# Kernel optimization log

Hardware: AMD Instinct MI355X
Metric: run time of the kernel (lower is better)

## Reference

```python
import jax, jax.numpy as jnp
import numpy as np
from jax import lax

VOL, PATCH, DIM, DEPTH, HEADS, DIM_HEAD, MLP, CH, B = 64, 8, 768, 4, 12, 64, 3072, 1, 2
INNER = HEADS * DIM_HEAD
GS = VOL // PATCH              # 8 -> N = 512 tokens
EPS = 1e-5


def _sincos_1d(embed_dim, pos):
    omega = np.arange(embed_dim // 2, dtype=float) / (embed_dim / 2.0)
    omega = 1.0 / 10000 ** omega
    out = np.einsum('m,d->md', pos.reshape(-1), omega)
    return np.concatenate([np.sin(out), np.cos(out)], axis=1)


def _pos_embed_3d(embed_dim, gs):
    gd = np.arange(gs, dtype=np.float32)
    gh = np.arange(gs, dtype=np.float32)
    gw = np.arange(gs, dtype=np.float32)
    grid = np.stack(np.meshgrid(gw, gh, gd), axis=0).reshape([3, 1, gs, gs, gs])
    emb = np.concatenate([_sincos_1d(embed_dim // 3, grid[i]) for i in range(3)], axis=1)
    return jnp.asarray(emb, jnp.float32)[None]  # [1, N, dim]


def setup_inputs() -> dict:
    key = jax.random.key(0)
    ks = jax.random.split(key, 12)
    s = 0.02  # xavier-like small init scale
    d = {
        'volume': jax.random.normal(ks[0], (B, CH, VOL, VOL, VOL), jnp.float32),
        'conv_w': jax.random.normal(ks[1], (DIM, CH, PATCH, PATCH, PATCH), jnp.float32) * s,
        'conv_b': jnp.zeros((DIM,), jnp.float32),
        'pos_embed': _pos_embed_3d(DIM, GS),
        'ln1_w': jnp.ones((DEPTH, DIM), jnp.float32),
        'ln1_b': jnp.zeros((DEPTH, DIM), jnp.float32),
        'w_qkv': jax.random.normal(ks[2], (DEPTH, DIM, 3 * INNER), jnp.float32) * s,
        'w_o': jax.random.normal(ks[3], (DEPTH, INNER, DIM), jnp.float32) * s,
        'b_o': jnp.zeros((DEPTH, DIM), jnp.float32),
        'ln2_w': jnp.ones((DEPTH, DIM), jnp.float32),
        'ln2_b': jnp.zeros((DEPTH, DIM), jnp.float32),
        'w1': jax.random.normal(ks[4], (DEPTH, DIM, MLP), jnp.float32) * s,
        'b1': jnp.zeros((DEPTH, MLP), jnp.float32),
        'w2': jax.random.normal(ks[5], (DEPTH, MLP, DIM), jnp.float32) * s,
        'b2': jnp.zeros((DEPTH, DIM), jnp.float32),
        'lnf_w': jnp.ones((DIM,), jnp.float32),
        'lnf_b': jnp.zeros((DIM,), jnp.float32),
    }
    return d


def _ln(x, w, b):
    m = jnp.mean(x, axis=-1, keepdims=True)
    v = jnp.mean(jnp.square(x - m), axis=-1, keepdims=True)
    return (x - m) * lax.rsqrt(v + EPS) * w + b


def _forward(volume, conv_w, conv_b, pos_embed, ln1_w, ln1_b, w_qkv, w_o, b_o,
             ln2_w, ln2_b, w1, b1, w2, b2, lnf_w, lnf_b):
    # Conv3d patch embedding (stride == kernel == patch)
    x = lax.conv_general_dilated(volume, conv_w, window_strides=(PATCH,) * 3,
                                 padding='VALID',
                                 dimension_numbers=('NCDHW', 'OIDHW', 'NCDHW'))
    x = x + conv_b[None, :, None, None, None]
    b = x.shape[0]
    x = x.reshape(b, DIM, -1).transpose(0, 2, 1)   # b (d h w) c -> [B, N, dim]
    x = x + pos_embed
    scale = DIM_HEAD ** -0.5

    def layer(x, p):
        l1w, l1b, wqkv, wo, bo, l2w, l2b, W1, B1, W2, B2 = p
        h = _ln(x, l1w, l1b)
        qkv = h @ wqkv                               # [B, N, 3*inner]
        q, k, v = jnp.split(qkv, 3, axis=-1)
        def heads(t):
            bsz, n, _ = t.shape
            return t.reshape(bsz, n, HEADS, DIM_HEAD).transpose(0, 2, 1, 3)
        q, k, v = heads(q), heads(k), heads(v)
        attn = jax.nn.softmax(jnp.einsum('bhqd,bhkd->bhqk', q, k) * scale, axis=-1)
        o = jnp.einsum('bhqk,bhkd->bhqd', attn, v)   # [B, H, N, dh]
        o = o.transpose(0, 2, 1, 3).reshape(x.shape[0], -1, INNER)
        x = x + (o @ wo + bo)
        h = _ln(x, l2w, l2b)
        x = x + (jnp.tanh(h @ W1 + B1) @ W2 + B2)
        return x, None

    params = (ln1_w, ln1_b, w_qkv, w_o, b_o, ln2_w, ln2_b, w1, b1, w2, b2)
    x, _ = lax.scan(layer, x, params)
    return _ln(x, lnf_w, lnf_b)


def reference(volume, conv_w, conv_b, pos_embed, ln1_w, ln1_b, w_qkv, w_o, b_o,
              ln2_w, ln2_b, w1, b1, w2, b2, lnf_w, lnf_b):
    return _forward(volume, conv_w, conv_b, pos_embed, ln1_w, ln1_b, w_qkv, w_o, b_o,
                    ln2_w, ln2_b, w1, b1, w2, b2, lnf_w, lnf_b)
```

## Files before the change

kernel.cpp:

```cpp
#include <hip/hip_runtime.h>
#include <hip/hip_bf16.h>

typedef __hip_bfloat16 bf16;
typedef short bf16x8 __attribute__((ext_vector_type(8)));
typedef float f32x4 __attribute__((ext_vector_type(4)));

__device__ __forceinline__ float b2f(bf16 v) { return __bfloat162float(v); }
__device__ __forceinline__ void storev(float* p, float v) { *p = v; }
__device__ __forceinline__ void storev(bf16* p, float v) { *p = __float2bfloat16(v); }

__device__ __forceinline__ void gl2lds16(const bf16* g, bf16* l) {
  __builtin_amdgcn_global_load_lds(
      (const __attribute__((address_space(1))) unsigned int*)g,
      (__attribute__((address_space(3))) unsigned int*)l, 16, 0, 0);
}

__global__ void im2col_kernel(const float* __restrict__ vol, bf16* __restrict__ out) {
  int t = blockIdx.x;
  int b = t >> 9, n = t & 511;
  int pd = n >> 6, ph = (n >> 3) & 7, pw = n & 7;
  const float* vb = vol + ((size_t)b << 18);
  for (int l = threadIdx.x; l < 512; l += 256) {
    int i = l >> 6, j = (l >> 3) & 7, k = l & 7;
    out[(size_t)t * 512 + l] =
        __float2bfloat16(vb[(pd * 8 + i) * 4096 + (ph * 8 + j) * 64 + (pw * 8 + k)]);
  }
}

__global__ void convert_kernel(const float* __restrict__ in, bf16* __restrict__ out, int n) {
  int i = (blockIdx.x * 256 + threadIdx.x) * 4;
  if (i + 3 < n) {
    float4 v = *(const float4*)&in[i];
    out[i + 0] = __float2bfloat16(v.x);
    out[i + 1] = __float2bfloat16(v.y);
    out[i + 2] = __float2bfloat16(v.z);
    out[i + 3] = __float2bfloat16(v.w);
  }
}

__global__ __launch_bounds__(256) void transpose_all(
    const float* __restrict__ wqkv, const float* __restrict__ wo,
    const float* __restrict__ w1, const float* __restrict__ w2,
    bf16* __restrict__ tqkv, bf16* __restrict__ two,
    bf16* __restrict__ t1, bf16* __restrict__ t2) {
  int bid = blockIdx.x;
  size_t L = blockIdx.y;
  const float* in;
  bf16* out;
  int R, C, tc, t0;
  if (bid < 432)       { in = wqkv + L * 768 * 2304; out = tqkv + L * 768 * 2304; R = 768;  C = 2304; tc = 36; t0 = bid; }
  else if (bid < 576)  { in = wo + L * 768 * 768;    out = two + L * 768 * 768;   R = 768;  C = 768;  tc = 12; t0 = bid - 432; }
  else if (bid < 1152) { in = w1 + L * 768 * 3072;   out = t1 + L * 768 * 3072;   R = 768;  C = 3072; tc = 48; t0 = bid - 576; }
  else                 { in = w2 + L * 3072 * 768;   out = t2 + L * 3072 * 768;   R = 3072; C = 768;  tc = 12; t0 = bid - 1152; }
  int r0 = (t0 / tc) * 64, c0 = (t0 % tc) * 64;
  __shared__ float tile[64][65];
  int tx = threadIdx.x & 15, ty = threadIdx.x >> 4;
#pragma unroll
  for (int yy = 0; yy < 4; ++yy) {
    float4 v = *(const float4*)&in[(size_t)(r0 + ty + yy * 16) * C + c0 + tx * 4];
    tile[ty + yy * 16][tx * 4 + 0] = v.x;
    tile[ty + yy * 16][tx * 4 + 1] = v.y;
    tile[ty + yy * 16][tx * 4 + 2] = v.z;
    tile[ty + yy * 16][tx * 4 + 3] = v.w;
  }
  __syncthreads();
  int cl = threadIdx.x >> 3;
  int rb = (threadIdx.x & 7) * 8;
#pragma unroll
  for (int half = 0; half < 2; ++half) {
    int c = cl + half * 32;
    bf16 pk[8];
#pragma unroll
    for (int e = 0; e < 8; ++e) pk[e] = __float2bfloat16(tile[rb + e][c]);
    *(uint4*)&out[(size_t)(c0 + c) * R + r0 + rb] = *(uint4*)pk;
  }
}

template <typename OutT>
__global__ void ln_kernel(const float* __restrict__ x, const float* __restrict__ w,
                          const float* __restrict__ b, OutT* __restrict__ out) {
  int row = blockIdx.x, tid = threadIdx.x;
  const float* xr = x + (size_t)row * 768;
  float s = 0.f, ss = 0.f;
  for (int i = tid; i < 768; i += 256) { float v = xr[i]; s += v; ss += v * v; }
  for (int off = 32; off; off >>= 1) {
    s += __shfl_xor(s, off);
    ss += __shfl_xor(ss, off);
  }
  __shared__ float sb[4], ssb[4];
  int wid = tid >> 6;
  if ((tid & 63) == 0) { sb[wid] = s; ssb[wid] = ss; }
  __syncthreads();
  s = sb[0] + sb[1] + sb[2] + sb[3];
  ss = ssb[0] + ssb[1] + ssb[2] + ssb[3];
  float m = s * (1.f / 768.f);
  float var = ss * (1.f / 768.f) - m * m;
  float r = rsqrtf(var + 1e-5f);
  for (int i = tid; i < 768; i += 256)
    storev(out + (size_t)row * 768 + i, (xr[i] - m) * r * w[i] + b[i]);
}

template <int BM, int BN, int EPI>
__global__ __launch_bounds__(256) void mfma_gemm(
    const bf16* __restrict__ A, const bf16* __restrict__ Bt,
    const float* __restrict__ bias, const float* __restrict__ aux,
    bf16* __restrict__ vt,
    void* __restrict__ Cout, int M, int N, int K) {
  constexpr int WTM = BM / 2, WTN = BN / 2;
  constexpr int MT = WTM / 16, NT = WTN / 16;
  __shared__ bf16 As[BM * 64];
  __shared__ bf16 Bs[BN * 64];
  int tid = threadIdx.x;
  int wave = tid >> 6, lane = tid & 63;
  int wm = wave >> 1, wn = wave & 1;
  int m15 = lane & 15, q = lane >> 4;
  int m0 = blockIdx.y * BM, n0 = blockIdx.x * BN;
  int kspan = K / gridDim.z;
  int kbeg = blockIdx.z * kspan, kend = kbeg + kspan;

  f32x4 acc[MT][NT];
#pragma unroll
  for (int i = 0; i < MT; ++i)
#pragma unroll
    for (int j = 0; j < NT; ++j) acc[i][j] = (f32x4){0.f, 0.f, 0.f, 0.f};

  for (int k0 = kbeg; k0 < kend; k0 += 64) {
#pragma unroll
    for (int it = 0; it < BM * 8 / 256; ++it) {
      int c = tid + it * 256;
      int row = c >> 3, cc = c & 7;
      gl2lds16(&A[(size_t)(m0 + row) * K + k0 + cc * 8], &As[c * 8]);
    }
#pragma unroll
    for (int it = 0; it < BN * 8 / 256; ++it) {
      int c = tid + it * 256;
      int row = c >> 3, cc = c & 7;
      gl2lds16(&Bt[(size_t)(n0 + row) * K + k0 + cc * 8], &Bs[c * 8]);
    }
    __syncthreads();
#pragma unroll
    for (int s = 0; s < 2; ++s) {
      bf16x8 af[MT], bfr[NT];
#pragma unroll
      for (int i = 0; i < MT; ++i)
        af[i] = *(const bf16x8*)&As[(wm * WTM + i * 16 + m15) * 64 + s * 32 + q * 8];
#pragma unroll
      for (int j = 0; j < NT; ++j)
        bfr[j] = *(const bf16x8*)&Bs[(wn * WTN + j * 16 + m15) * 64 + s * 32 + q * 8];
#pragma unroll
      for (int i = 0; i < MT; ++i)
#pragma unroll
        for (int j = 0; j < NT; ++j)
          acc[i][j] = __builtin_amdgcn_mfma_f32_16x16x32_bf16(af[i], bfr[j], acc[i][j], 0, 0, 0);
    }
    __syncthreads();
  }

#pragma unroll
  for (int i = 0; i < MT; ++i) {
#pragma unroll
    for (int j = 0; j < NT; ++j) {
      int col = n0 + wn * WTN + j * 16 + m15;
      if (EPI == 4) {
        if (col < 1536) {
#pragma unroll
          for (int r = 0; r < 4; ++r) {
            int row = m0 + wm * WTM + i * 16 + q * 4 + r;
            ((bf16*)Cout)[(size_t)row * 1536 + col] = __float2bfloat16(acc[i][j][r]);
          }
        } else {
          int row0 = m0 + wm * WTM + i * 16 + q * 4;
          int cl = col - 1536;
          int hh = cl >> 6, dd = cl & 63;
          int bb = row0 >> 9, tok = row0 & 511;
          bf16 pk[4];
#pragma unroll
          for (int r = 0; r < 4; ++r) pk[r] = __float2bfloat16(acc[i][j][r]);
          *(uint2*)&vt[((size_t)(bb * 12 + hh) * 64 + dd) * 512 + tok] = *(uint2*)pk;
        }
      } else if (EPI == 5) {
        float bv = (blockIdx.z == 0) ? bias[col] : 0.f;
#pragma unroll
        for (int r = 0; r < 4; ++r) {
          int row = m0 + wm * WTM + i * 16 + q * 4 + r;
          unsafeAtomicAdd(&((float*)Cout)[(size_t)row * N + col], acc[i][j][r] + bv);
        }
      } else {
        float bv = (EPI == 0) ? 0.f : bias[col];
#pragma unroll
        for (int r = 0; r < 4; ++r) {
          int row = m0 + wm * WTM + i * 16 + q * 4 + r;
          float v = acc[i][j][r] + bv;
          if (EPI == 2) v = tanhf(v);
          if (EPI == 3) v += aux[(size_t)(row & 511) * N + col];
          if (EPI == 0 || EPI == 2)
            ((bf16*)Cout)[(size_t)row * N + col] = __float2bfloat16(v);
          else
            ((float*)Cout)[(size_t)row * N + col] = v;
        }
      }
    }
  }
}

__global__ __launch_bounds__(128) void attn_mfma(const bf16* __restrict__ qk,
                                                 const bf16* __restrict__ Vt,
                                                 bf16* __restrict__ o) {
  constexpr int PS = 520;
  __shared__ bf16 KVs[64 * 64];
  __shared__ bf16 P[32 * PS];
  int bh = blockIdx.x;
  int b = bh / 12, hh = bh % 12;
  int q0 = blockIdx.y * 32;
  int tid = threadIdx.x;
  int wave = tid >> 6, lane = tid & 63;
  int n15 = lane & 15, quad = lane >> 4;
  const bf16* qkb = qk + (size_t)b * 512 * 1536;
  int ql = wave * 16 + n15;

  const bf16* qp = qkb + (size_t)(q0 + ql) * 1536 + hh * 64 + quad * 8;
  bf16x8 qf0 = *(const bf16x8*)qp;
  bf16x8 qf1 = *(const bf16x8*)(qp + 32);

  f32x4 S[32];
#pragma unroll
  for (int i = 0; i < 32; ++i) S[i] = (f32x4){0.f, 0.f, 0.f, 0.f};

  const bf16* kbase = qkb + 768 + hh * 64;
#pragma unroll
  for (int kc = 0; kc < 8; ++kc) {
    __syncthreads();
#pragma unroll
    for (int it = 0; it < 4; ++it) {
      int c = tid + it * 128;
      int r = c >> 3, cc = c & 7;
      gl2lds16(&kbase[(size_t)(kc * 64 + r) * 1536 + cc * 8], &KVs[c * 8]);
    }
    __syncthreads();
#pragma unroll
    for (int t = 0; t < 4; ++t) {
      int idx = kc * 4 + t;
      bf16x8 a0 = *(const bf16x8*)&KVs[(t * 16 + n15) * 64 + quad * 8];
      bf16x8 a1 = *(const bf16x8*)&KVs[(t * 16 + n15) * 64 + 32 + quad * 8];
      S[idx] = __builtin_amdgcn_mfma_f32_16x16x32_bf16(a0, qf0, S[idx], 0, 0, 0);
      S[idx] = __builtin_amdgcn_mfma_f32_16x16x32_bf16(a1, qf1, S[idx], 0, 0, 0);
    }
  }

  float mx = -1e30f;
#pragma unroll
  for (int i = 0; i < 32; ++i)
#pragma unroll
    for (int r = 0; r < 4; ++r) { S[i][r] *= 0.125f; mx = fmaxf(mx, S[i][r]); }
  mx = fmaxf(mx, __shfl_xor(mx, 16));
  mx = fmaxf(mx, __shfl_xor(mx, 32));
  float sum = 0.f;
#pragma unroll
  for (int i = 0; i < 32; ++i)
#pragma unroll
    for (int r = 0; r < 4; ++r) { float e = __expf(S[i][r] - mx); S[i][r] = e; sum += e; }
  sum += __shfl_xor(sum, 16);
  sum += __shfl_xor(sum, 32);
  float inv = 1.f / sum;

#pragma unroll
  for (int i = 0; i < 32; ++i) {
    bf16 pk[4];
#pragma unroll
    for (int r = 0; r < 4; ++r) pk[r] = __float2bfloat16(S[i][r] * inv);
    *(uint2*)&P[(size_t)ql * PS + i * 16 + quad * 4] = *(uint2*)pk;
  }

  f32x4 oacc[4];
#pragma unroll
  for (int dt = 0; dt < 4; ++dt) oacc[dt] = (f32x4){0.f, 0.f, 0.f, 0.f};
  const bf16* vtb = Vt + (size_t)bh * 64 * 512;
  for (int kc = 0; kc < 8; ++kc) {
    __syncthreads();
#pragma unroll
    for (int it = 0; it < 4; ++it) {
      int c = tid + it * 128;
      int r = c >> 3, cc = c & 7;
      gl2lds16(&vtb[(size_t)r * 512 + kc * 64 + cc * 8], &KVs[c * 8]);
    }
    __syncthreads();
    bf16x8 p0 = *(const bf16x8*)&P[(size_t)ql * PS + kc * 64 + quad * 8];
    bf16x8 p1 = *(const bf16x8*)&P[(size_t)ql * PS + kc * 64 + 32 + quad * 8];
#pragma unroll
    for (int dt = 0; dt < 4; ++dt) {
      bf16x8 v0 = *(const bf16x8*)&KVs[(dt * 16 + n15) * 64 + quad * 8];
      bf16x8 v1 = *(const bf16x8*)&KVs[(dt * 16 + n15) * 64 + 32 + quad * 8];
      oacc[dt] = __builtin_amdgcn_mfma_f32_16x16x32_bf16(p0, v0, oacc[dt], 0, 0, 0);
      oacc[dt] = __builtin_amdgcn_mfma_f32_16x16x32_bf16(p1, v1, oacc[dt], 0, 0, 0);
    }
  }

#pragma unroll
  for (int dt = 0; dt < 4; ++dt)
#pragma unroll
    for (int r = 0; r < 4; ++r) {
      int tok = q0 + wave * 16 + quad * 4 + r;
      o[((size_t)b * 512 + tok) * 768 + hh * 64 + dt * 16 + n15] =
          __float2bfloat16(oacc[dt][r]);
    }
}

extern "C" void kernel_launch(void* const* d_in, const int* in_sizes, int n_in,
                              void* d_out, int out_size, void* d_ws, size_t ws_size,
                              hipStream_t stream) {
  const float* volume = (const float*)d_in[0];
  const float* conv_w = (const float*)d_in[1];
  const float* conv_b = (const float*)d_in[2];
  const float* pos    = (const float*)d_in[3];
  const float* ln1w   = (const float*)d_in[4];
  const float* ln1b   = (const float*)d_in[5];
  const float* wqkv   = (const float*)d_in[6];
  const float* wo     = (const float*)d_in[7];
  const float* bo     = (const float*)d_in[8];
  const float* ln2w   = (const float*)d_in[9];
  const float* ln2b   = (const float*)d_in[10];
  const float* w1     = (const float*)d_in[11];
  const float* b1     = (const float*)d_in[12];
  const float* w2     = (const float*)d_in[13];
  const float* b2     = (const float*)d_in[14];
  const float* lnfw   = (const float*)d_in[15];
  const float* lnfb   = (const float*)d_in[16];

  char* w = (char*)d_ws;
  float* x    = (float*)(w + 0);
  bf16* h     = (bf16*)(w + 3145728);
  bf16* qk    = (bf16*)(w + 4718592);
  bf16* patchA= qk;
  bf16* Vt    = (bf16*)(w + 7864320);
  bf16* oact  = (bf16*)(w + 9437184);
  bf16* cwb   = (bf16*)(w + 15728640);
  bf16* tqkv  = (bf16*)(w + 16515072);
  bf16* two   = (bf16*)(w + 30670848);
  bf16* t1    = (bf16*)(w + 35389440);
  bf16* t2    = (bf16*)(w + 54263808);

  convert_kernel<<<384, 256, 0, stream>>>(conv_w, cwb, 768 * 512);
  im2col_kernel<<<1024, 256, 0, stream>>>(volume, patchA);
  transpose_all<<<dim3(1728, 4), 256, 0, stream>>>(wqkv, wo, w1, w2, tqkv, two, t1, t2);
  mfma_gemm<64, 64, 3><<<dim3(12, 16), 256, 0, stream>>>(
      patchA, cwb, conv_b, pos, nullptr, x, 1024, 768, 512);

  for (int L = 0; L < 4; ++L) {
    ln_kernel<bf16><<<1024, 256, 0, stream>>>(x, ln1w + L * 768, ln1b + L * 768, h);
    mfma_gemm<64, 64, 4><<<dim3(36, 16), 256, 0, stream>>>(
        h, tqkv + (size_t)L * 768 * 2304, nullptr, nullptr, Vt, qk, 1024, 2304, 768);
    attn_mfma<<<dim3(24, 16), 128, 0, stream>>>(qk, Vt, oact);
    mfma_gemm<64, 64, 5><<<dim3(12, 16, 2), 256, 0, stream>>>(
        oact, two + (size_t)L * 768 * 768, bo + L * 768, nullptr, nullptr, x, 1024, 768, 768);
    ln_kernel<bf16><<<1024, 256, 0, stream>>>(x, ln2w + L * 768, ln2b + L * 768, h);
    mfma_gemm<64, 64, 2><<<dim3(48, 16), 256, 0, stream>>>(
        h, t1 + (size_t)L * 768 * 3072, b1 + L * 3072, nullptr, nullptr, oact, 1024, 3072, 768);
    mfma_gemm<64, 64, 5><<<dim3(12, 16, 4), 256, 0, stream>>>(
        oact, t2 + (size_t)L * 768 * 3072, b2 + L * 768, nullptr, nullptr, x, 1024, 768, 3072);
  }

  ln_kernel<float><<<1024, 256, 0, stream>>>(x, lnfw, lnfb, (float*)d_out);
}
```

Before: 519.5 us.

## Use one wave per row in LayerNorm, bf16 transpose tile, taller GEMM tiles

LayerNorm now assigns one 64-lane wave per row and holds the row in registers, which removes the shared-memory reduction, the block barrier and the second read of x. The weight transpose converts to bf16 before staging in LDS and writes 16 elements per thread, halving LDS traffic. The QKV and MLP-up GEMMs move to 128x64 tiles, halving the grid height for more reuse per block at the cost of fewer blocks.

```diff
diff --git a/kernel.cpp b/kernel.cpp
--- a/kernel.cpp
+++ b/kernel.cpp
@@ -53,51 +53,56 @@
   else if (bid < 1152) { in = w1 + L * 768 * 3072;   out = t1 + L * 768 * 3072;   R = 768;  C = 3072; tc = 48; t0 = bid - 576; }
   else                 { in = w2 + L * 3072 * 768;   out = t2 + L * 3072 * 768;   R = 3072; C = 768;  tc = 12; t0 = bid - 1152; }
   int r0 = (t0 / tc) * 64, c0 = (t0 % tc) * 64;
-  __shared__ float tile[64][65];
-  int tx = threadIdx.x & 15, ty = threadIdx.x >> 4;
+  __shared__ bf16 Ts[64 * 68];
+  int t = threadIdx.x;
+  int r = t >> 4, cq = t & 15;
 #pragma unroll
   for (int yy = 0; yy < 4; ++yy) {
-    float4 v = *(const float4*)&in[(size_t)(r0 + ty + yy * 16) * C + c0 + tx * 4];
-    tile[ty + yy * 16][tx * 4 + 0] = v.x;
-    tile[ty + yy * 16][tx * 4 + 1] = v.y;
-    tile[ty + yy * 16][tx * 4 + 2] = v.z;
-    tile[ty + yy * 16][tx * 4 + 3] = v.w;
+    int row = r + yy * 16;
+    float4 v = *(const float4*)&in[(size_t)(r0 + row) * C + c0 + cq * 4];
+    bf16 pk[4] = {__float2bfloat16(v.x), __float2bfloat16(v.y),
+                  __float2bfloat16(v.z), __float2bfloat16(v.w)};
+    *(uint2*)&Ts[row * 68 + cq * 4] = *(uint2*)pk;
   }
   __syncthreads();
-  int cl = threadIdx.x >> 3;
-  int rb = (threadIdx.x & 7) * 8;
-#pragma unroll
-  for (int half = 0; half < 2; ++half) {
-    int c = cl + half * 32;
-    bf16 pk[8];
-#pragma unroll
-    for (int e = 0; e < 8; ++e) pk[e] = __float2bfloat16(tile[rb + e][c]);
-    *(uint4*)&out[(size_t)(c0 + c) * R + r0 + rb] = *(uint4*)pk;
-  }
+  int oc = t >> 2, seg = t & 3;
+  bf16 pk[16];
+#pragma unroll
+  for (int j = 0; j < 16; ++j) {
+    int e = (j + seg * 4) & 15;
+    pk[e] = Ts[(seg * 16 + e) * 68 + oc];
+  }
+  *(uint4*)&out[(size_t)(c0 + oc) * R + r0 + seg * 16] = *(uint4*)&pk[0];
+  *(uint4*)&out[(size_t)(c0 + oc) * R + r0 + seg * 16 + 8] = *(uint4*)&pk[8];
 }
 
 template <typename OutT>
-__global__ void ln_kernel(const float* __restrict__ x, const float* __restrict__ w,
-                          const float* __restrict__ b, OutT* __restrict__ out) {
-  int row = blockIdx.x, tid = threadIdx.x;
+__global__ __launch_bounds__(256) void ln_kernel(const float* __restrict__ x,
+                                                 const float* __restrict__ w,
+                                                 const float* __restrict__ b,
+                                                 OutT* __restrict__ out) {
+  int row = blockIdx.x * 4 + (threadIdx.x >> 6);
+  int lane = threadIdx.x & 63;
   const float* xr = x + (size_t)row * 768;
+  float v[12];
   float s = 0.f, ss = 0.f;
-  for (int i = tid; i < 768; i += 256) { float v = xr[i]; s += v; ss += v * v; }
+#pragma unroll
+  for (int i = 0; i < 12; ++i) {
+    v[i] = xr[lane + i * 64];
+    s += v[i];
+    ss += v[i] * v[i];
+  }
   for (int off = 32; off; off >>= 1) {
     s += __shfl_xor(s, off);
     ss += __shfl_xor(ss, off);
   }
-  __shared__ float sb[4], ssb[4];
-  int wid = tid >> 6;
-  if ((tid & 63) == 0) { sb[wid] = s; ssb[wid] = ss; }
-  __syncthreads();
-  s = sb[0] + sb[1] + sb[2] + sb[3];
-  ss = ssb[0] + ssb[1] + ssb[2] + ssb[3];
   float m = s * (1.f / 768.f);
   float var = ss * (1.f / 768.f) - m * m;
-  float r = rsqrtf(var + 1e-5f);
-  for (int i = tid; i < 768; i += 256)
-    storev(out + (size_t)row * 768 + i, (xr[i] - m) * r * w[i] + b[i]);
+  float rr = rsqrtf(var + 1e-5f);
+#pragma unroll
+  for (int i = 0; i < 12; ++i)
+    storev(out + (size_t)row * 768 + lane + i * 64,
+           (v[i] - m) * rr * w[lane + i * 64] + b[lane + i * 64]);
 }
 
 template <int BM, int BN, int EPI>
@@ -346,18 +351,18 @@
       patchA, cwb, conv_b, pos, nullptr, x, 1024, 768, 512);
 
   for (int L = 0; L < 4; ++L) {
-    ln_kernel<bf16><<<1024, 256, 0, stream>>>(x, ln1w + L * 768, ln1b + L * 768, h);
-    mfma_gemm<64, 64, 4><<<dim3(36, 16), 256, 0, stream>>>(
+    ln_kernel<bf16><<<256, 256, 0, stream>>>(x, ln1w + L * 768, ln1b + L * 768, h);
+    mfma_gemm<128, 64, 4><<<dim3(36, 8), 256, 0, stream>>>(
         h, tqkv + (size_t)L * 768 * 2304, nullptr, nullptr, Vt, qk, 1024, 2304, 768);
     attn_mfma<<<dim3(24, 16), 128, 0, stream>>>(qk, Vt, oact);
     mfma_gemm<64, 64, 5><<<dim3(12, 16, 2), 256, 0, stream>>>(
         oact, two + (size_t)L * 768 * 768, bo + L * 768, nullptr, nullptr, x, 1024, 768, 768);
-    ln_kernel<bf16><<<1024, 256, 0, stream>>>(x, ln2w + L * 768, ln2b + L * 768, h);
-    mfma_gemm<64, 64, 2><<<dim3(48, 16), 256, 0, stream>>>(
+    ln_kernel<bf16><<<256, 256, 0, stream>>>(x, ln2w + L * 768, ln2b + L * 768, h);
+    mfma_gemm<128, 64, 2><<<dim3(48, 8), 256, 0, stream>>>(
         h, t1 + (size_t)L * 768 * 3072, b1 + L * 3072, nullptr, nullptr, oact, 1024, 3072, 768);
     mfma_gemm<64, 64, 5><<<dim3(12, 16, 4), 256, 0, stream>>>(
         oact, t2 + (size_t)L * 768 * 3072, b2 + L * 768, nullptr, nullptr, x, 1024, 768, 3072);
   }
 
-  ln_kernel<float><<<1024, 256, 0, stream>>>(x, lnfw, lnfb, (float*)d_out);
-}
+  ln_kernel<float><<<256, 256, 0, stream>>>(x, lnfw, lnfb, (float*)d_out);
+}
```

New measurement: 556.0 us. 7.0% more time.
